# Optimization experiments

Hardware: AMD Instinct MI355X
Metric: run time of the kernel (lower is better)

## Reference

```python
import jax, jax.numpy as jnp
import numpy as np

LEAKY_SLOPE = 0.05


def setup_inputs() -> dict:
    key = jax.random.key(0)
    k1, k2, k3, k4, k5 = jax.random.split(key, 5)
    N, E, F, H = 50000, 1600000, 256, 64
    x = jax.random.normal(k1, (N, F), dtype=jnp.float32)
    edge_index = jax.random.randint(k2, (2, E), 0, N, dtype=jnp.int64)
    fc_w = jax.random.normal(k3, (H, F), dtype=jnp.float32) * 0.05
    a_w = jax.random.normal(k4, (2 * H,), dtype=jnp.float32) * 0.05
    a_b = jax.random.normal(k5, (1,), dtype=jnp.float32) * 0.05
    return {"x": x, "edge_index": edge_index, "fc_w": fc_w, "a_w": a_w, "a_b": a_b}


def reference(x, edge_index, fc_w, a_w, a_b):
    N = x.shape[0]
    H = fc_w.shape[0]
    src = edge_index[0]
    dst = edge_index[1]
    # z = fc(x), no bias: [N, H]
    z = x @ fc_w.T
    # attention logits per edge; cat([z_i, z_j]) @ a_w == z_i @ a_w[:H] + z_j @ a_w[H:]
    z_j = z[dst]                      # [E, H] gathered destination features
    e = z[src] @ a_w[:H] + z_j @ a_w[H:] + a_b[0]   # [E]
    h = jnp.exp(jax.nn.leaky_relu(e, negative_slope=LEAKY_SLOPE))
    # segment softmax over edges grouped by source node (as in original scatter_add)
    h_sum = jax.ops.segment_sum(h, src, num_segments=N)   # [N]
    alpha = h / h_sum[src]                                 # [E]
    # sparse mm: out[i] = sum_{edges with src=i} alpha_e * z[dst_e]
    out = jax.ops.segment_sum(alpha[:, None] * z_j, src, num_segments=N)  # [N, H]
    return out, alpha
```

## Files before the change

kernel.cpp:

```cpp
#include <hip/hip_runtime.h>
#include <hip/hip_bf16.h>
#include <cstdint>
#include <cstddef>


constexpr int FDIM = 256;
constexpr int HDIM = 64;
constexpr float LEAKY = 0.05f;

typedef __attribute__((ext_vector_type(8))) short short8v;
typedef __attribute__((ext_vector_type(4))) float f32x4;

__device__ __forceinline__ short bfs(float f) {
  return (short)__builtin_bit_cast(unsigned short, __float2bfloat16(f));
}
__device__ __forceinline__ short8v cvt8(float4 lo, float4 hi) {
  short8v r;
  r[0] = bfs(lo.x); r[1] = bfs(lo.y); r[2] = bfs(lo.z); r[3] = bfs(lo.w);
  r[4] = bfs(hi.x); r[5] = bfs(hi.y); r[6] = bfs(hi.z); r[7] = bfs(hi.w);
  return r;
}

__global__ __launch_bounds__(256) void k_wt(
    const float* __restrict__ fcw, short* __restrict__ wb)
{
  const int t = blockIdx.x * 256 + threadIdx.x;
  const int f = t >> 6;
  const int lane = t & 63;
  const int ks = f >> 2, cb = f & 3;
  const int col = cb * 16 + (lane & 15);
  const int kb = ks * 32 + (lane >> 4) * 8;
  short8v v;
  #pragma unroll
  for (int j = 0; j < 8; ++j) v[j] = bfs(fcw[col * FDIM + kb + j]);
  reinterpret_cast<short8v*>(wb)[t] = v;
}

__global__ __launch_bounds__(256) void k_fcm(
    const float* __restrict__ x, const short* __restrict__ wb,
    const float* __restrict__ aw,
    unsigned short* __restrict__ zb, float* __restrict__ s1,
    float* __restrict__ s2, int N)
{
  __shared__ __align__(16) unsigned short zt[128 * 72];

  const int tid = threadIdx.x;
  const int lane = tid & 63;
  const int wave = tid >> 6;
  const int n0 = blockIdx.x * 128;
  const int rb = n0 + wave * 32;
  const int l4 = lane >> 4;
  const int lm = lane & 15;

  f32x4 acc[2][4] = {};

  const int r0c = min(rb + lm, N - 1);
  const int r1c = min(rb + 16 + lm, N - 1);
  const float* xp0 = x + (size_t)r0c * FDIM + l4 * 8;
  const float* xp1 = x + (size_t)r1c * FDIM + l4 * 8;
  const short8v* wbv = reinterpret_cast<const short8v*>(wb);

  #pragma unroll
  for (int ks = 0; ks < 8; ++ks) {
    const float4 a0l = *reinterpret_cast<const float4*>(xp0 + ks * 32);
    const float4 a0h = *reinterpret_cast<const float4*>(xp0 + ks * 32 + 4);
    const float4 a1l = *reinterpret_cast<const float4*>(xp1 + ks * 32);
    const float4 a1h = *reinterpret_cast<const float4*>(xp1 + ks * 32 + 4);
    const short8v fa0 = cvt8(a0l, a0h);
    const short8v fa1 = cvt8(a1l, a1h);
    #pragma unroll
    for (int cb = 0; cb < 4; ++cb) {
      const short8v fb = wbv[(ks * 4 + cb) * 64 + lane];
      acc[0][cb] = __builtin_amdgcn_mfma_f32_16x16x32_bf16(fa0, fb, acc[0][cb], 0, 0, 0);
      acc[1][cb] = __builtin_amdgcn_mfma_f32_16x16x32_bf16(fa1, fb, acc[1][cb], 0, 0, 0);
    }
  }

  float aw1l[4], aw2l[4];
  #pragma unroll
  for (int cb = 0; cb < 4; ++cb) {
    aw1l[cb] = aw[cb * 16 + lm];
    aw2l[cb] = aw[HDIM + cb * 16 + lm];
  }
  #pragma unroll
  for (int mb = 0; mb < 2; ++mb) {
    const int rloc = rb + mb * 16 + l4 * 4;
    #pragma unroll
    for (int reg = 0; reg < 4; ++reg) {
      float t1 = 0.f, t2 = 0.f;
      #pragma unroll
      for (int cb = 0; cb < 4; ++cb) {
        t1 = fmaf(acc[mb][cb][reg], aw1l[cb], t1);
        t2 = fmaf(acc[mb][cb][reg], aw2l[cb], t2);
      }
      #pragma unroll
      for (int off = 1; off < 16; off <<= 1) {
        t1 += __shfl_xor(t1, off, 64);
        t2 += __shfl_xor(t2, off, 64);
      }
      if (lm == reg && rloc + reg < N) {
        s1[rloc + reg] = t1;
        s2[rloc + reg] = t2;
      }
    }
  }

  #pragma unroll
  for (int mb = 0; mb < 2; ++mb)
    #pragma unroll
    for (int cb = 0; cb < 4; ++cb)
      #pragma unroll
      for (int reg = 0; reg < 4; ++reg) {
        const int rl = wave * 32 + mb * 16 + l4 * 4 + reg;
        zt[rl * 72 + cb * 16 + lm] =
            (unsigned short)__builtin_bit_cast(unsigned short,
                __float2bfloat16(acc[mb][cb][reg]));
      }
  __syncthreads();
  const int row = tid >> 1, hf = tid & 1;
  const int n = n0 + row;
  if (n < N) {
    const uint4* s = reinterpret_cast<const uint4*>(&zt[row * 72 + hf * 32]);
    uint4 v0 = s[0], v1 = s[1], v2 = s[2], v3 = s[3];
    uint4* d = reinterpret_cast<uint4*>(zb + (size_t)n * HDIM + hf * 32);
    d[0] = v0; d[1] = v1; d[2] = v2; d[3] = v3;
  }
}

__global__ __launch_bounds__(1024) void k_b1(
    const int* __restrict__ src, unsigned int* __restrict__ hist,
    int E, int nB, int nCh, int chunkLg)
{
  __shared__ unsigned int lh[256];
  const int tid = threadIdx.x;
  if (tid < 256) lh[tid] = 0;
  __syncthreads();
  const int e0 = blockIdx.x << chunkLg;
  const int e1 = min(e0 + (1 << chunkLg), E);
  for (int e = e0 + tid; e < e1; e += 1024)
    atomicAdd(&lh[src[e] >> 8], 1u);
  __syncthreads();
  if (tid < nB) hist[(size_t)tid * nCh + blockIdx.x] = lh[tid];
}

__global__ __launch_bounds__(256) void k_bsum(
    unsigned int* __restrict__ hist, unsigned int* __restrict__ tot,
    int nB, int nCh)
{
  const int b = blockIdx.x * 4 + (threadIdx.x >> 6);
  const int lane = threadIdx.x & 63;
  if (b >= nB) return;
  unsigned int* row = hist + (size_t)b * nCh;
  unsigned int running = 0;
  for (int j = 0; j < nCh; j += 64) {
    const int c = j + lane;
    unsigned int v = (c < nCh) ? row[c] : 0;
    unsigned int s = v;
    #pragma unroll
    for (int off = 1; off < 64; off <<= 1) {
      unsigned int t = __shfl_up(s, off, 64);
      if (lane >= off) s += t;
    }
    if (c < nCh) row[c] = running + s - v;
    running += __shfl(s, 63, 64);
  }
  if (lane == 0) tot[b] = running;
}

__global__ __launch_bounds__(256) void k_bscan2(
    const unsigned int* __restrict__ tot, int* __restrict__ bucket_base,
    int nB, int E)
{
  __shared__ unsigned int part[256];
  const int t = threadIdx.x;
  const unsigned int v = (t < nB) ? tot[t] : 0;
  part[t] = v;
  __syncthreads();
  for (int off = 1; off < 256; off <<= 1) {
    unsigned int u = (t >= off) ? part[t - off] : 0;
    __syncthreads();
    part[t] += u;
    __syncthreads();
  }
  if (t < nB) bucket_base[t] = (int)(part[t] - v);
  if (t == 0) bucket_base[nB] = E;
}

__global__ __launch_bounds__(1024) void k_b2(
    const int* __restrict__ src, const int* __restrict__ dst,
    const unsigned int* __restrict__ hist, const int* __restrict__ bucket_base,
    unsigned int* __restrict__ bucketed, int E, int nB, int nCh, int chunkLg)
{
  __shared__ unsigned int staged[8192];
  __shared__ unsigned int gbase[256];
  __shared__ unsigned int lhist[256];
  __shared__ unsigned int lbase[256];
  __shared__ unsigned int lcur[256];
  __shared__ unsigned int part[256];

  const int tid = threadIdx.x;
  const int c = blockIdx.x;
  if (tid < 256) lhist[tid] = 0;
  if (tid < nB)
    gbase[tid] = (unsigned int)bucket_base[tid] + hist[(size_t)tid * nCh + c];
  __syncthreads();

  const int e0 = c << chunkLg;
  const int e1 = min(e0 + (1 << chunkLg), E);
  const int csize = e1 - e0;

  for (int e = e0 + tid; e < e1; e += 1024)
    atomicAdd(&lhist[src[e] >> 8], 1u);
  __syncthreads();

  if (tid < 256) part[tid] = lhist[tid];
  __syncthreads();
  for (int off = 1; off < 256; off <<= 1) {
    unsigned int t = (tid < 256 && tid >= off) ? part[tid - off] : 0;
    __syncthreads();
    if (tid < 256) part[tid] += t;
    __syncthreads();
  }
  if (tid < 256) {
    lbase[tid] = part[tid] - lhist[tid];
    lcur[tid] = lbase[tid];
  }
  __syncthreads();

  for (int e = e0 + tid; e < e1; e += 1024) {
    const unsigned int s = (unsigned int)src[e];
    const unsigned int pos = atomicAdd(&lcur[s >> 8], 1u);
    staged[pos] = (s << 16) | (unsigned int)dst[e];
  }
  __syncthreads();

  for (int i = tid; i < csize; i += 1024) {
    const unsigned int v = staged[i];
    const unsigned int b = v >> 24;
    bucketed[gbase[b] + ((unsigned int)i - lbase[b])] = v;
  }
}

__global__ __launch_bounds__(1024) void k_b3(
    const unsigned int* __restrict__ bucketed, const int* __restrict__ bucket_base,
    int* __restrict__ rowptr, unsigned short* __restrict__ csr_dst,
    int nB, int N, int E)
{
  __shared__ unsigned short staged[16384];
  __shared__ unsigned int lh[256];
  __shared__ unsigned int part[256];
  __shared__ unsigned int cur[256];

  const int b = blockIdx.x;
  const int tid = threadIdx.x;
  const int seg0 = bucket_base[b];
  const int seg1 = bucket_base[b + 1];
  const int len = seg1 - seg0;
  if (tid < 256) lh[tid] = 0;
  __syncthreads();

  for (int j = seg0 + tid; j < seg1; j += 1024)
    atomicAdd(&lh[(bucketed[j] >> 16) & 0xFFu], 1u);
  __syncthreads();

  if (tid < 256) part[tid] = lh[tid];
  __syncthreads();
  for (int off = 1; off < 256; off <<= 1) {
    unsigned int t = (tid < 256 && tid >= off) ? part[tid - off] : 0;
    __syncthreads();
    if (tid < 256) part[tid] += t;
    __syncthreads();
  }
  if (tid < 256) {
    const unsigned int base = part[tid] - lh[tid];
    cur[tid] = base;
    const int n = b * 256 + tid;
    if (n < N) rowptr[n] = seg0 + (int)base;
  }
  if (b == nB - 1 && tid == 0) rowptr[N] = E;
  __syncthreads();

  if (len <= 16384) {
    for (int j = seg0 + tid; j < seg1; j += 1024) {
      const unsigned int v = bucketed[j];
      const unsigned int pos = atomicAdd(&cur[(v >> 16) & 0xFFu], 1u);
      staged[pos] = (unsigned short)(v & 0xFFFFu);
    }
    __syncthreads();
    for (int i = tid; i < len; i += 1024)
      csr_dst[seg0 + i] = staged[i];
  } else {
    for (int j = seg0 + tid; j < seg1; j += 1024) {
      const unsigned int v = bucketed[j];
      const unsigned int pos = atomicAdd(&cur[(v >> 16) & 0xFFu], 1u);
      csr_dst[seg0 + pos] = (unsigned short)(v & 0xFFFFu);
    }
  }
}

__global__ __launch_bounds__(256) void k_node(
    const unsigned short* __restrict__ csr_dst, const int* __restrict__ rowptr,
    const float* __restrict__ s1, const float* __restrict__ s2,
    const float* __restrict__ ab, const unsigned short* __restrict__ zb,
    float* __restrict__ out, float* __restrict__ rinv, int N)
{
  __shared__ float hbuf[4][64];
  __shared__ int   dbuf[4][64];

  const int wave = threadIdx.x >> 6;
  const int node = blockIdx.x * 4 + wave;
  const int lane = threadIdx.x & 63;
  if (node >= N) return;
  const int r0 = rowptr[node];
  const int r1 = rowptr[node + 1];
  if (r1 == r0) {
    out[(size_t)node * HDIM + lane] = 0.f;
    if (lane == 0) rinv[node] = 0.f;
    return;
  }
  const float s1n = s1[node];
  const float b = ab[0];
  const int half = lane >> 5;
  const int fp = (lane & 31) << 1;
  float ax = 0.f, ay = 0.f, hs = 0.f;
  float* hb = hbuf[wave];
  int*   db = dbuf[wave];

  for (int base = r0; base < r1; base += 64) {
    const int j = base + lane;
    float h = 0.f;
    int dl = 0;
    if (j < r1) {
      dl = (int)csr_dst[j];
      float v = s1n + s2[dl] + b;
      v = v > 0.f ? v : LEAKY * v;
      h = __expf(v);
    }
    hs += h;
    hb[lane] = h;
    db[lane] = dl;
    const int cnt = min(64, r1 - base);
    const int pairs = (cnt + 1) >> 1;
    int t = 0;
    for (; t + 4 <= pairs; t += 4) {
      const int i0 = 2 * t + half;
      const float h0 = hb[i0],     h1 = hb[i0 + 2];
      const float h2 = hb[i0 + 4], h3 = hb[i0 + 6];
      const int   d0 = db[i0],     d1 = db[i0 + 2];
      const int   d2 = db[i0 + 4], d3 = db[i0 + 6];
      const unsigned int w0 = *reinterpret_cast<const unsigned int*>(zb + (size_t)d0 * HDIM + fp);
      const unsigned int w1 = *reinterpret_cast<const unsigned int*>(zb + (size_t)d1 * HDIM + fp);
      const unsigned int w2 = *reinterpret_cast<const unsigned int*>(zb + (size_t)d2 * HDIM + fp);
      const unsigned int w3 = *reinterpret_cast<const unsigned int*>(zb + (size_t)d3 * HDIM + fp);
      ax = fmaf(h0, __uint_as_float(w0 << 16), ax);
      ay = fmaf(h0, __uint_as_float(w0 & 0xffff0000u), ay);
      ax = fmaf(h1, __uint_as_float(w1 << 16), ax);
      ay = fmaf(h1, __uint_as_float(w1 & 0xffff0000u), ay);
      ax = fmaf(h2, __uint_as_float(w2 << 16), ax);
      ay = fmaf(h2, __uint_as_float(w2 & 0xffff0000u), ay);
      ax = fmaf(h3, __uint_as_float(w3 << 16), ax);
      ay = fmaf(h3, __uint_as_float(w3 & 0xffff0000u), ay);
    }
    for (; t < pairs; ++t) {
      const int i0 = 2 * t + half;
      const float hB = hb[i0];
      const int   dB = db[i0];
      const unsigned int w = *reinterpret_cast<const unsigned int*>(zb + (size_t)dB * HDIM + fp);
      ax = fmaf(hB, __uint_as_float(w << 16), ax);
      ay = fmaf(hB, __uint_as_float(w & 0xffff0000u), ay);
    }
  }
  #pragma unroll
  for (int off = 32; off > 0; off >>= 1) hs += __shfl_xor(hs, off, 64);
  ax += __shfl_xor(ax, 32, 64);
  ay += __shfl_xor(ay, 32, 64);
  const float inv = 1.0f / hs;
  if (lane < 32) {
    float2 o = {ax * inv, ay * inv};
    *reinterpret_cast<float2*>(out + (size_t)node * HDIM + fp) = o;
    if (lane == 0) rinv[node] = inv;
  }
}

__global__ __launch_bounds__(256) void k_alpha(
    const int* __restrict__ src, const int* __restrict__ dst,
    const float* __restrict__ s1, const float* __restrict__ s2,
    const float* __restrict__ ab, const float* __restrict__ rinv,
    float* __restrict__ alpha, int E)
{
  int e = blockIdx.x * blockDim.x + threadIdx.x;
  if (e >= E) return;
  const int s = src[e];
  float v = s1[s] + s2[dst[e]] + ab[0];
  v = v > 0.f ? v : LEAKY * v;
  alpha[e] = __expf(v) * rinv[s];
}

extern "C" void kernel_launch(void* const* d_in, const int* in_sizes, int n_in,
                              void* d_out, int out_size, void* d_ws, size_t ws_size,
                              hipStream_t stream) {
  const int E  = in_sizes[1] / 2;
  const int H2 = in_sizes[3];
  const int Hh = H2 / 2;
  const int Ff = in_sizes[2] / Hh;
  const int N  = in_sizes[0] / Ff;

  const float* x   = (const float*)d_in[0];
  const int*   ei  = (const int*)d_in[1];
  const float* fcw = (const float*)d_in[2];
  const float* aw  = (const float*)d_in[3];
  const float* ab  = (const float*)d_in[4];
  const int* src = ei;
  const int* dst = ei + E;

  float* out   = (float*)d_out;
  float* alpha = out + (size_t)N * HDIM;

  const int nB = (N + 255) >> 8;
  int chunkLg = 13;
  while (((E + (1 << chunkLg) - 1) >> chunkLg) > 256) ++chunkLg;
  const int nCh = (E + (1 << chunkLg) - 1) >> chunkLg;

  unsigned short* zb = (unsigned short*)d_ws;
  float* s1   = (float*)(zb + (size_t)N * HDIM);
  float* s2   = s1 + N;
  float* rinv = s2 + N;
  short* wb   = (short*)(rinv + N);
  int* rowptr = (int*)(wb + 8 * 4 * 64 * 8);
  int* bucket_base = rowptr + (N + 1);
  unsigned int* tot = (unsigned int*)(bucket_base + (nB + 2));
  unsigned int* bucketed = tot + 256;
  unsigned int* hist = bucketed + E;
  unsigned short* csr_dst = (unsigned short*)(hist + (size_t)nB * nCh);

  k_wt<<<8, 256, 0, stream>>>(fcw, wb);
  k_fcm<<<(N + 127) / 128, 256, 0, stream>>>(x, wb, aw, zb, s1, s2, N);

  k_b1<<<nCh, 1024, 0, stream>>>(src, hist, E, nB, nCh, chunkLg);
  k_bsum<<<(nB + 3) / 4, 256, 0, stream>>>(hist, tot, nB, nCh);
  k_bscan2<<<1, 256, 0, stream>>>(tot, bucket_base, nB, E);
  k_b2<<<nCh, 1024, 0, stream>>>(src, dst, hist, bucket_base, bucketed,
                                 E, nB, nCh, chunkLg);
  k_b3<<<nB, 1024, 0, stream>>>(bucketed, bucket_base, rowptr, csr_dst, nB, N, E);

  k_node<<<(N + 3) / 4, 256, 0, stream>>>(
      csr_dst, rowptr, s1, s2, ab, zb, out, rinv, N);

  const int eb = (E + 255) / 256;
  k_alpha<<<eb, 256, 0, stream>>>(src, dst, s1, s2, ab, rinv, alpha, E);
}
```

Before: 105.4 us.

## Reuse local bucket offsets, widen node gathers, and pair-process alpha edges

k_b1 now computes each chunk's exclusive local prefix scan and stores it, so k_b2 no longer re-reads src to rebuild the local histogram and scan. k_node switches from 2-feature-per-lane pair gathers to 4-feature uint2 gathers, with four edges processed in parallel per wave and an extra shuffle reduction. k_alpha handles two edges per thread with vectorized int2 index loads and float2 stores. These cut a redundant pass over src and raise per-load width, at the cost of extra workspace and more shuffles per node.

```diff
diff --git a/kernel.cpp b/kernel.cpp
--- a/kernel.cpp
+++ b/kernel.cpp
@@ -20,6 +20,8 @@
   r[4] = bfs(hi.x); r[5] = bfs(hi.y); r[6] = bfs(hi.z); r[7] = bfs(hi.w);
   return r;
 }
+__device__ __forceinline__ float blo(unsigned int w) { return __uint_as_float(w << 16); }
+__device__ __forceinline__ float bhi(unsigned int w) { return __uint_as_float(w & 0xffff0000u); }
 
 __global__ __launch_bounds__(256) void k_wt(
     const float* __restrict__ fcw, short* __restrict__ wb)
@@ -129,9 +131,10 @@
 
 __global__ __launch_bounds__(1024) void k_b1(
     const int* __restrict__ src, unsigned int* __restrict__ hist,
-    int E, int nB, int nCh, int chunkLg)
+    unsigned int* __restrict__ lbs, int E, int nB, int nCh, int chunkLg)
 {
   __shared__ unsigned int lh[256];
+  __shared__ unsigned int part[256];
   const int tid = threadIdx.x;
   if (tid < 256) lh[tid] = 0;
   __syncthreads();
@@ -140,7 +143,18 @@
   for (int e = e0 + tid; e < e1; e += 1024)
     atomicAdd(&lh[src[e] >> 8], 1u);
   __syncthreads();
-  if (tid < nB) hist[(size_t)tid * nCh + blockIdx.x] = lh[tid];
+  if (tid < 256) part[tid] = lh[tid];
+  __syncthreads();
+  for (int off = 1; off < 256; off <<= 1) {
+    unsigned int t = (tid < 256 && tid >= off) ? part[tid - off] : 0;
+    __syncthreads();
+    if (tid < 256) part[tid] += t;
+    __syncthreads();
+  }
+  if (tid < nB) {
+    hist[(size_t)tid * nCh + blockIdx.x] = lh[tid];
+    lbs[(size_t)blockIdx.x * 256 + tid] = part[tid] - lh[tid];
+  }
 }
 
 __global__ __launch_bounds__(256) void k_bsum(
@@ -188,44 +202,28 @@
 
 __global__ __launch_bounds__(1024) void k_b2(
     const int* __restrict__ src, const int* __restrict__ dst,
-    const unsigned int* __restrict__ hist, const int* __restrict__ bucket_base,
+    const unsigned int* __restrict__ hist, const unsigned int* __restrict__ lbs,
+    const int* __restrict__ bucket_base,
     unsigned int* __restrict__ bucketed, int E, int nB, int nCh, int chunkLg)
 {
   __shared__ unsigned int staged[8192];
   __shared__ unsigned int gbase[256];
-  __shared__ unsigned int lhist[256];
   __shared__ unsigned int lbase[256];
   __shared__ unsigned int lcur[256];
-  __shared__ unsigned int part[256];
 
   const int tid = threadIdx.x;
   const int c = blockIdx.x;
-  if (tid < 256) lhist[tid] = 0;
-  if (tid < nB)
+  if (tid < nB) {
     gbase[tid] = (unsigned int)bucket_base[tid] + hist[(size_t)tid * nCh + c];
+    const unsigned int lb = lbs[(size_t)c * 256 + tid];
+    lbase[tid] = lb;
+    lcur[tid] = lb;
+  }
   __syncthreads();
 
   const int e0 = c << chunkLg;
   const int e1 = min(e0 + (1 << chunkLg), E);
   const int csize = e1 - e0;
-
-  for (int e = e0 + tid; e < e1; e += 1024)
-    atomicAdd(&lhist[src[e] >> 8], 1u);
-  __syncthreads();
-
-  if (tid < 256) part[tid] = lhist[tid];
-  __syncthreads();
-  for (int off = 1; off < 256; off <<= 1) {
-    unsigned int t = (tid < 256 && tid >= off) ? part[tid - off] : 0;
-    __syncthreads();
-    if (tid < 256) part[tid] += t;
-    __syncthreads();
-  }
-  if (tid < 256) {
-    lbase[tid] = part[tid] - lhist[tid];
-    lcur[tid] = lbase[tid];
-  }
-  __syncthreads();
 
   for (int e = e0 + tid; e < e1; e += 1024) {
     const unsigned int s = (unsigned int)src[e];
@@ -313,6 +311,8 @@
   if (node >= N) return;
   const int r0 = rowptr[node];
   const int r1 = rowptr[node + 1];
+  const int q  = lane >> 4;
+  const int f4 = (lane & 15) << 2;
   if (r1 == r0) {
     out[(size_t)node * HDIM + lane] = 0.f;
     if (lane == 0) rinv[node] = 0.f;
@@ -320,9 +320,7 @@
   }
   const float s1n = s1[node];
   const float b = ab[0];
-  const int half = lane >> 5;
-  const int fp = (lane & 31) << 1;
-  float ax = 0.f, ay = 0.f, hs = 0.f;
+  float a0 = 0.f, a1 = 0.f, a2 = 0.f, a3 = 0.f, hs = 0.f;
   float* hb = hbuf[wave];
   int*   db = dbuf[wave];
 
@@ -340,44 +338,44 @@
     hb[lane] = h;
     db[lane] = dl;
     const int cnt = min(64, r1 - base);
-    const int pairs = (cnt + 1) >> 1;
+    const int quads = (cnt + 3) >> 2;
     int t = 0;
-    for (; t + 4 <= pairs; t += 4) {
-      const int i0 = 2 * t + half;
-      const float h0 = hb[i0],     h1 = hb[i0 + 2];
-      const float h2 = hb[i0 + 4], h3 = hb[i0 + 6];
-      const int   d0 = db[i0],     d1 = db[i0 + 2];
-      const int   d2 = db[i0 + 4], d3 = db[i0 + 6];
-      const unsigned int w0 = *reinterpret_cast<const unsigned int*>(zb + (size_t)d0 * HDIM + fp);
-      const unsigned int w1 = *reinterpret_cast<const unsigned int*>(zb + (size_t)d1 * HDIM + fp);
-      const unsigned int w2 = *reinterpret_cast<const unsigned int*>(zb + (size_t)d2 * HDIM + fp);
-      const unsigned int w3 = *reinterpret_cast<const unsigned int*>(zb + (size_t)d3 * HDIM + fp);
-      ax = fmaf(h0, __uint_as_float(w0 << 16), ax);
-      ay = fmaf(h0, __uint_as_float(w0 & 0xffff0000u), ay);
-      ax = fmaf(h1, __uint_as_float(w1 << 16), ax);
-      ay = fmaf(h1, __uint_as_float(w1 & 0xffff0000u), ay);
-      ax = fmaf(h2, __uint_as_float(w2 << 16), ax);
-      ay = fmaf(h2, __uint_as_float(w2 & 0xffff0000u), ay);
-      ax = fmaf(h3, __uint_as_float(w3 << 16), ax);
-      ay = fmaf(h3, __uint_as_float(w3 & 0xffff0000u), ay);
-    }
-    for (; t < pairs; ++t) {
-      const int i0 = 2 * t + half;
-      const float hB = hb[i0];
-      const int   dB = db[i0];
-      const unsigned int w = *reinterpret_cast<const unsigned int*>(zb + (size_t)dB * HDIM + fp);
-      ax = fmaf(hB, __uint_as_float(w << 16), ax);
-      ay = fmaf(hB, __uint_as_float(w & 0xffff0000u), ay);
+    for (; t + 2 <= quads; t += 2) {
+      const int i0 = 4 * t + q, i1 = i0 + 4;
+      const float h0 = hb[i0], h1 = hb[i1];
+      const int   d0 = db[i0], d1 = db[i1];
+      const uint2 w0 = *reinterpret_cast<const uint2*>(zb + (size_t)d0 * HDIM + f4);
+      const uint2 w1 = *reinterpret_cast<const uint2*>(zb + (size_t)d1 * HDIM + f4);
+      a0 = fmaf(h0, blo(w0.x), a0);
+      a1 = fmaf(h0, bhi(w0.x), a1);
+      a2 = fmaf(h0, blo(w0.y), a2);
+      a3 = fmaf(h0, bhi(w0.y), a3);
+      a0 = fmaf(h1, blo(w1.x), a0);
+      a1 = fmaf(h1, bhi(w1.x), a1);
+      a2 = fmaf(h1, blo(w1.y), a2);
+      a3 = fmaf(h1, bhi(w1.y), a3);
+    }
+    for (; t < quads; ++t) {
+      const int i0 = 4 * t + q;
+      const float h0 = hb[i0];
+      const int   d0 = db[i0];
+      const uint2 w0 = *reinterpret_cast<const uint2*>(zb + (size_t)d0 * HDIM + f4);
+      a0 = fmaf(h0, blo(w0.x), a0);
+      a1 = fmaf(h0, bhi(w0.x), a1);
+      a2 = fmaf(h0, blo(w0.y), a2);
+      a3 = fmaf(h0, bhi(w0.y), a3);
     }
   }
   #pragma unroll
   for (int off = 32; off > 0; off >>= 1) hs += __shfl_xor(hs, off, 64);
-  ax += __shfl_xor(ax, 32, 64);
-  ay += __shfl_xor(ay, 32, 64);
+  a0 += __shfl_xor(a0, 16, 64); a1 += __shfl_xor(a1, 16, 64);
+  a2 += __shfl_xor(a2, 16, 64); a3 += __shfl_xor(a3, 16, 64);
+  a0 += __shfl_xor(a0, 32, 64); a1 += __shfl_xor(a1, 32, 64);
+  a2 += __shfl_xor(a2, 32, 64); a3 += __shfl_xor(a3, 32, 64);
   const float inv = 1.0f / hs;
-  if (lane < 32) {
-    float2 o = {ax * inv, ay * inv};
-    *reinterpret_cast<float2*>(out + (size_t)node * HDIM + fp) = o;
+  if (lane < 16) {
+    float4 o = {a0 * inv, a1 * inv, a2 * inv, a3 * inv};
+    *reinterpret_cast<float4*>(out + (size_t)node * HDIM + f4) = o;
     if (lane == 0) rinv[node] = inv;
   }
 }
@@ -388,12 +386,24 @@
     const float* __restrict__ ab, const float* __restrict__ rinv,
     float* __restrict__ alpha, int E)
 {
-  int e = blockIdx.x * blockDim.x + threadIdx.x;
+  const int e = (blockIdx.x * blockDim.x + threadIdx.x) * 2;
   if (e >= E) return;
-  const int s = src[e];
-  float v = s1[s] + s2[dst[e]] + ab[0];
-  v = v > 0.f ? v : LEAKY * v;
-  alpha[e] = __expf(v) * rinv[s];
+  const float bb = ab[0];
+  if (e + 1 < E) {
+    const int2 sv = *reinterpret_cast<const int2*>(src + e);
+    const int2 dv = *reinterpret_cast<const int2*>(dst + e);
+    float v0 = s1[sv.x] + s2[dv.x] + bb;
+    float v1 = s1[sv.y] + s2[dv.y] + bb;
+    v0 = v0 > 0.f ? v0 : LEAKY * v0;
+    v1 = v1 > 0.f ? v1 : LEAKY * v1;
+    float2 o = {__expf(v0) * rinv[sv.x], __expf(v1) * rinv[sv.y]};
+    *reinterpret_cast<float2*>(alpha + e) = o;
+  } else {
+    const int s = src[e];
+    float v = s1[s] + s2[dst[e]] + bb;
+    v = v > 0.f ? v : LEAKY * v;
+    alpha[e] = __expf(v) * rinv[s];
+  }
 }
 
 extern "C" void kernel_launch(void* const* d_in, const int* in_sizes, int n_in,
@@ -431,21 +441,22 @@
   unsigned int* tot = (unsigned int*)(bucket_base + (nB + 2));
   unsigned int* bucketed = tot + 256;
   unsigned int* hist = bucketed + E;
-  unsigned short* csr_dst = (unsigned short*)(hist + (size_t)nB * nCh);
+  unsigned int* lbs = hist + (size_t)nB * nCh;
+  unsigned short* csr_dst = (unsigned short*)(lbs + (size_t)nCh * 256);
 
   k_wt<<<8, 256, 0, stream>>>(fcw, wb);
   k_fcm<<<(N + 127) / 128, 256, 0, stream>>>(x, wb, aw, zb, s1, s2, N);
 
-  k_b1<<<nCh, 1024, 0, stream>>>(src, hist, E, nB, nCh, chunkLg);
+  k_b1<<<nCh, 1024, 0, stream>>>(src, hist, lbs, E, nB, nCh, chunkLg);
   k_bsum<<<(nB + 3) / 4, 256, 0, stream>>>(hist, tot, nB, nCh);
   k_bscan2<<<1, 256, 0, stream>>>(tot, bucket_base, nB, E);
-  k_b2<<<nCh, 1024, 0, stream>>>(src, dst, hist, bucket_base, bucketed,
+  k_b2<<<nCh, 1024, 0, stream>>>(src, dst, hist, lbs, bucket_base, bucketed,
                                  E, nB, nCh, chunkLg);
   k_b3<<<nB, 1024, 0, stream>>>(bucketed, bucket_base, rowptr, csr_dst, nB, N, E);
 
   k_node<<<(N + 3) / 4, 256, 0, stream>>>(
       csr_dst, rowptr, s1, s2, ab, zb, out, rinv, N);
 
-  const int eb = (E + 255) / 256;
+  const int eb = (E + 511) / 512;
   k_alpha<<<eb, 256, 0, stream>>>(src, dst, s1, s2, ab, rinv, alpha, E);
 }
```

New measurement: 109.3 us. 1.04x slower.
